# Optimization experiments

Measured on AMD Instinct MI355X. Metric: run time of the kernel, lower is better.

The kernel has to match this reference:

```python
import jax, jax.numpy as jnp
import numpy as np

D_MODEL = 96
D_STATE = 6
D_CONV = 9
D_INNER = 2 * D_MODEL          # expand = 2
DT_RANK = (D_MODEL + 15) // 16  # ceil(d_model/16) = 6
DIM_IN = 64
DIM_OUT = 64
BATCH = 16
SEQLEN = 4096


def setup_inputs() -> dict:
    key = jax.random.key(0)
    ks = jax.random.split(key, 12)
    def s(k, shape, scale=0.02):
        return jax.random.normal(k, shape, jnp.float32) * scale
    return {
        "x": jax.random.normal(ks[0], (BATCH, SEQLEN, D_MODEL), jnp.float32),
        # Mamba block params
        "in_proj_w": s(ks[1], (2 * D_INNER, D_MODEL)),
        "conv_w": s(ks[2], (D_INNER, D_CONV), 0.1),   # depthwise conv kernel
        "conv_b": jnp.zeros((D_INNER,), jnp.float32),
        "x_proj_w": s(ks[3], (DT_RANK + 2 * D_STATE, D_INNER)),
        "dt_proj_w": s(ks[4], (D_INNER, DT_RANK), 0.1),
        "dt_proj_b": s(ks[5], (D_INNER,), 0.1),
        "A_log": jnp.log(jnp.tile(jnp.arange(1, D_STATE + 1, dtype=jnp.float32), (D_INNER, 1))),
        "D_param": jnp.ones((D_INNER,), jnp.float32),
        "out_proj_w": s(ks[6], (D_MODEL, D_INNER)),
        "norm_w": jnp.ones((D_MODEL,), jnp.float32),  # RMSNorm weight
        # heads
        "out_fc_w": s(ks[7], (DIM_IN, D_MODEL)),
        "out_fc_b": jnp.zeros((DIM_IN,), jnp.float32),
        "mu_w": s(ks[8], (DIM_OUT, DIM_IN)),
        "mu_b": jnp.zeros((DIM_OUT,), jnp.float32),
        "sigma_w": s(ks[9], (DIM_OUT, DIM_IN)),
        "sigma_b": jnp.zeros((DIM_OUT,), jnp.float32),
    }


def _mamba_block(x, in_proj_w, conv_w, conv_b, x_proj_w, dt_proj_w, dt_proj_b,
                 A_log, D_param, out_proj_w):
    Bsz = x.shape[0]
    xz = jnp.einsum('bld,ed->ble', x, in_proj_w)          # (B,L,2*ED)
    xs, z = jnp.split(xz, 2, axis=-1)
    # causal depthwise conv1d (torch pads d_conv-1 both sides then trims right)
    xt = xs.transpose(0, 2, 1)                            # (B,ED,L)
    kern = conv_w[:, None, :]                             # (ED,1,K)
    xc = jax.lax.conv_general_dilated(xt, kern, window_strides=(1,),
                                      padding=[(D_CONV - 1, 0)],
                                      feature_group_count=D_INNER)
    xc = (xc + conv_b[None, :, None]).transpose(0, 2, 1)  # (B,L,ED)
    xc = jax.nn.silu(xc)
    dbc = jnp.einsum('ble,fe->blf', xc, x_proj_w)         # (B,L,dt_rank+2N)
    delta_r = dbc[..., :DT_RANK]
    Bm = dbc[..., DT_RANK:DT_RANK + D_STATE]              # (B,L,N)
    Cm = dbc[..., DT_RANK + D_STATE:]                     # (B,L,N)
    delta = jax.nn.softplus(jnp.einsum('blr,er->ble', delta_r, dt_proj_w) + dt_proj_b)
    A = -jnp.exp(A_log)                                   # (ED,N)
    deltaA = jnp.exp(delta[..., None] * A)                # (B,L,ED,N)
    BX = (delta * xc)[..., None] * Bm[:, :, None, :]      # (B,L,ED,N)

    def step(h, inputs):
        dA, bx = inputs
        h = dA * h + bx
        return h, h

    h0 = jnp.zeros((Bsz, D_INNER, D_STATE), x.dtype)
    _, hs = jax.lax.scan(step, h0, (deltaA.swapaxes(0, 1), BX.swapaxes(0, 1)))
    y = jnp.einsum('lben,bln->ble', hs, Cm)               # (B,L,ED)
    y = y + D_param * xc
    y = y * jax.nn.silu(z)
    return jnp.einsum('ble,de->bld', y, out_proj_w)       # (B,L,D)


def reference(x, in_proj_w, conv_w, conv_b, x_proj_w, dt_proj_w, dt_proj_b,
              A_log, D_param, out_proj_w, norm_w,
              out_fc_w, out_fc_b, mu_w, mu_b, sigma_w, sigma_b):
    # residual block: x + mixer(RMSNorm(x))   (dropout is identity at eval)
    h = x * jax.lax.rsqrt(jnp.mean(x * x, axis=-1, keepdims=True) + 1e-5) * norm_w
    out = x + _mamba_block(h, in_proj_w, conv_w, conv_b, x_proj_w,
                           dt_proj_w, dt_proj_b, A_log, D_param, out_proj_w)
    e = out.mean(axis=1)                                  # (B,D)
    feat = jax.nn.elu(jnp.tanh(e @ out_fc_w.T + out_fc_b))
    mu = feat @ mu_w.T + mu_b
    sigma = jax.nn.elu(feat @ sigma_w.T + sigma_b) + 1.0 + 1e-14
    return (feat, mu, sigma)
```

## Files before the change

kernel.cpp:

```cpp
#include <hip/hip_runtime.h>
#include <math.h>

#define BATCH 16
#define SEQLEN 4096
#define D_MODEL 96
#define D_STATE 6
#define D_CONV 9
#define D_INNER 192
#define DT_RANK 6
#define NPOS (BATCH * SEQLEN)

#define NC2 128
#define CT2 (SEQLEN / NC2)
#define NSEG 16
#define CPS (NC2 / NSEG)

#define OFF_XS    0L
#define OFF_Z     (OFF_XS   + (long)NPOS * 96)
#define OFF_OUT4  (OFF_Z    + (long)NPOS * 96)
#define OFF_SEG   (OFF_OUT4 + (long)BATCH * NC2 * 5 * 192 * 4)
#define OFF_XPART (OFF_SEG  + (long)BATCH * NSEG * 5 * 192 * 4)

typedef short v8s __attribute__((ext_vector_type(8)));
typedef float v4f __attribute__((ext_vector_type(4)));

__device__ __forceinline__ float silu_fast(float v) {
    return __fdividef(v, 1.0f + __expf(-v));
}
__device__ __forceinline__ float softplus_fast(float v) {
    return (v > 20.0f) ? v : __logf(1.0f + __expf(v));
}
__device__ __forceinline__ float eluf(float v) {
    return (v > 0.0f) ? v : expm1f(v);
}
__device__ __forceinline__ unsigned int pack_bf16(float a, float b) {
    unsigned int ua = __float_as_uint(a), ub = __float_as_uint(b);
    ua += 0x7FFFu + ((ua >> 16) & 1u);
    ub += 0x7FFFu + ((ub >> 16) & 1u);
    return (ua >> 16) | (ub & 0xFFFF0000u);
}
__device__ __forceinline__ unsigned short bf16h(float v) {
    unsigned int u = __float_as_uint(v);
    u += 0x7FFFu + ((u >> 16) & 1u);
    return (unsigned short)(u >> 16);
}
__device__ __forceinline__ float bf2f(unsigned short h) {
    return __uint_as_float(((unsigned int)h) << 16);
}

#define TP1 64
__global__ __launch_bounds__(256, 2) void k1_rmsnorm_inproj(
    const float* __restrict__ x, const float* __restrict__ W,
    const float* __restrict__ norm_w,
    unsigned short* __restrict__ xs, unsigned short* __restrict__ z,
    float* __restrict__ xpart)
{
    __shared__ unsigned int s_ovl[7680];
    __shared__ unsigned int s_hA[64 * 52];
    __shared__ float s_part[TP1][4];
    __shared__ float s_scale[TP1];
    float* hRow = (float*)s_ovl;
    unsigned int* WB = s_ovl;

    const int tid = threadIdx.x;
    const long p0 = (long)blockIdx.x * TP1;

    {
        const float4* x4 = (const float4*)&x[p0 * 96];
        for (int i = tid; i < TP1 * 24; i += 256) {
            int p = i / 24, dq = i - p * 24;
            float4 v = x4[i];
            float* hr = &hRow[p * 101 + dq * 4];
            hr[0] = v.x; hr[1] = v.y; hr[2] = v.z; hr[3] = v.w;
        }
    }
    __syncthreads();

    {
        int p = tid >> 2, g = tid & 3;
        float ss = 0.0f;
        for (int d = g; d < 96; d += 4) { float v = hRow[p * 101 + d]; ss += v * v; }
        s_part[p][g] = ss;
    }
    __syncthreads();

    if (tid < TP1) {
        float ss = s_part[tid][0] + s_part[tid][1] + s_part[tid][2] + s_part[tid][3];
        s_scale[tid] = 1.0f / sqrtf(ss / 96.0f + 1e-5f);
    } else if (tid < TP1 + 96) {
        int d = tid - TP1;
        float s = 0.0f;
        for (int p = 0; p < TP1; p++) s += hRow[p * 101 + d];
        xpart[(long)blockIdx.x * 96 + d] = s;
    }
    __syncthreads();

    {
        const float2* nw2 = (const float2*)norm_w;
        for (int i = tid; i < TP1 * 48; i += 256) {
            int p = i / 48, dp = i - p * 48;
            float sc = s_scale[p];
            float2 nv = nw2[dp];
            float v0 = hRow[p * 101 + 2 * dp]     * sc * nv.x;
            float v1 = hRow[p * 101 + 2 * dp + 1] * sc * nv.y;
            s_hA[p * 52 + dp] = pack_bf16(v0, v1);
        }
    }

    const int wave = tid >> 6, lane = tid & 63;
    const int quad = lane >> 4, ln = lane & 15;
    const int n0 = wave * 96;

    v4f acc[4][6];
#pragma unroll
    for (int mt = 0; mt < 4; mt++)
#pragma unroll
        for (int nt = 0; nt < 6; nt++) acc[mt][nt] = (v4f){0.f, 0.f, 0.f, 0.f};

    for (int kc = 0; kc < 3; kc++) {
        __syncthreads();
        for (int i = tid; i < 384 * 16; i += 256) {
            int j = i >> 4, kp = i & 15;
            const float2 wv = *(const float2*)&W[j * 96 + kc * 32 + 2 * kp];
            WB[j * 20 + kp] = pack_bf16(wv.x, wv.y);
        }
        __syncthreads();

        v8s bfh[4];
#pragma unroll
        for (int mt = 0; mt < 4; mt++)
            bfh[mt] = *(const v8s*)&s_hA[(mt * 16 + ln) * 52 + kc * 16 + quad * 4];
#pragma unroll
        for (int nt = 0; nt < 6; nt++) {
            v8s aw = *(const v8s*)&WB[(n0 + nt * 16 + ln) * 20 + quad * 4];
#pragma unroll
            for (int mt = 0; mt < 4; mt++)
                acc[mt][nt] = __builtin_amdgcn_mfma_f32_16x16x32_bf16(
                    aw, bfh[mt], acc[mt][nt], 0, 0, 0);
        }
    }

    unsigned short* dst = (wave < 2) ? xs : z;
    const int jb = (wave & 1) * 96;
#pragma unroll
    for (int mt = 0; mt < 4; mt++) {
        long pos = p0 + mt * 16 + ln;
#pragma unroll
        for (int nt = 0; nt < 6; nt++) {
            uint2 v;
            v.x = pack_bf16(acc[mt][nt][0], acc[mt][nt][1]);
            v.y = pack_bf16(acc[mt][nt][2], acc[mt][nt][3]);
            *(uint2*)&dst[pos * D_INNER + jb + nt * 16 + quad * 4] = v;
        }
    }
}

#define SXSTR 200
__global__ __launch_bounds__(192, 4) void k2f_conv_scan(
    const unsigned short* __restrict__ xs, const unsigned short* __restrict__ z,
    const float* __restrict__ conv_w, const float* __restrict__ conv_b,
    const float* __restrict__ x_proj_w,
    const float* __restrict__ dt_w, const float* __restrict__ dt_b,
    const float* __restrict__ A_log, const float* __restrict__ D_param,
    float4* __restrict__ out4)
{
    __shared__ unsigned short sxc[CT2 * SXSTR];
    __shared__ unsigned short sxpB[18 * SXSTR];
    __shared__ float sMeta[CT2][20];
    const int e = threadIdx.x;
    const int c = blockIdx.x & (NC2 - 1);
    const int b = blockIdx.x >> 7;
    const int l0 = c * CT2;
    const long brow = (long)b * SEQLEN;

    {
        unsigned int* xpB = (unsigned int*)sxpB;
        for (int i = e; i < 18 * 96; i += 192) {
            int f = i / 96, kp = i - f * 96;
            const float2 wv = *(const float2*)&x_proj_w[f * 192 + 2 * kp];
            xpB[f * 100 + kp] = pack_bf16(wv.x, wv.y);
        }
    }

    float cw[D_CONV];
#pragma unroll
    for (int k = 0; k < D_CONV; k++) cw[k] = conv_w[e * D_CONV + k];
    const float cb = conv_b[e];
    float win[D_CONV];
#pragma unroll
    for (int k = 0; k < 8; k++) {
        int ll = l0 - 8 + k;
        win[k] = (ll >= 0) ? bf2f(xs[(brow + ll) * D_INNER + e]) : 0.0f;
    }
#pragma unroll
    for (int r = 0; r < CT2; r++) {
        win[8] = bf2f(xs[(brow + l0 + r) * D_INNER + e]);
        float s = cb;
#pragma unroll
        for (int k = 0; k < D_CONV; k++) s += win[k] * cw[k];
        sxc[r * SXSTR + e] = bf16h(silu_fast(s));
#pragma unroll
        for (int k = 0; k < 8; k++) win[k] = win[k + 1];
    }

    const unsigned short* zp = &z[(brow + l0) * D_INNER + e];
    float zv[CT2];
#pragma unroll
    for (int t = 0; t < CT2; t++) zv[t] = bf2f(zp[(long)t * D_INNER]);
    __syncthreads();

    {
        const int wave = e >> 6, lane = e & 63;
        const int quad = lane >> 4, ln = lane & 15;
        if (wave < 2) {
            const int mt = wave;
            const int r1 = (ln < 2) ? 16 + ln : 0;
            v4f dacc[2];
            dacc[0] = (v4f){0.f, 0.f, 0.f, 0.f};
            dacc[1] = (v4f){0.f, 0.f, 0.f, 0.f};
#pragma unroll
            for (int kc = 0; kc < 6; kc++) {
                v8s af  = *(const v8s*)&sxc[(mt * 16 + ln) * SXSTR + kc * 32 + quad * 8];
                v8s bf0 = *(const v8s*)&sxpB[ln * SXSTR + kc * 32 + quad * 8];
                v8s bf1 = *(const v8s*)&sxpB[r1 * SXSTR + kc * 32 + quad * 8];
                dacc[0] = __builtin_amdgcn_mfma_f32_16x16x32_bf16(af, bf0, dacc[0], 0, 0, 0);
                dacc[1] = __builtin_amdgcn_mfma_f32_16x16x32_bf16(af, bf1, dacc[1], 0, 0, 0);
            }
#pragma unroll
            for (int nt = 0; nt < 2; nt++) {
                int f = nt * 16 + ln;
                if (f < 18) {
                    int col = (f < 6) ? f : f + 2;
#pragma unroll
                    for (int r = 0; r < 4; r++)
                        sMeta[mt * 16 + quad * 4 + r][col] = dacc[nt][r];
                }
            }
        }
    }
    __syncthreads();

    float a[D_STATE];
#pragma unroll
    for (int n = 0; n < D_STATE; n++) a[n] = -__expf(A_log[e * D_STATE + n]);
    float dtw[DT_RANK];
#pragma unroll
    for (int q = 0; q < DT_RANK; q++) dtw[q] = dt_w[e * DT_RANK + q];
    const float dtb = dt_b[e];
    const float Dv = D_param[e];
    const float a0 = a[0];

    bool pok = true;
#pragma unroll
    for (int n = 1; n < D_STATE; n++)
        pok = pok && (fabsf(a[n] - (float)(n + 1) * a0)
                      <= 1e-4f * (float)(n + 1) * fabsf(a0));
    unsigned long long pmask = __ballot(pok);

    float S[D_STATE], G[D_STATE];
#pragma unroll
    for (int n = 0; n < D_STATE; n++) { S[n] = 0.0f; G[n] = 0.0f; }
    float ysum0 = 0.0f;

    if (pmask == 0xFFFFFFFFFFFFFFFFull) {
        float Pa = 1.0f;
#pragma unroll 2
        for (int t = 0; t < CT2; t++) {
            const float4* m4 = (const float4*)&sMeta[t][0];
            float4 m0 = m4[0], m1 = m4[1], mB0 = m4[2], mB1 = m4[3], mC = m4[4];
            float Bv[6] = {mB0.x, mB0.y, mB0.z, mB0.w, mB1.x, mB1.y};
            float Cv[6] = {mB1.z, mB1.w, mC.x, mC.y, mC.z, mC.w};
            float dr = dtb + m0.x * dtw[0] + m0.y * dtw[1] + m0.z * dtw[2]
                     + m0.w * dtw[3] + m1.x * dtw[4] + m1.y * dtw[5];
            float dl = softplus_fast(dr);
            float xv = bf2f(sxc[t * SXSTR + e]);
            float zw = silu_fast(zv[t]);
            float dx = dl * xv;
            float y = Dv * xv;
            float E = __expf(dl * a0);
            Pa *= E;
            float dA = E, Pn = Pa;
#pragma unroll
            for (int n = 0; n < D_STATE; n++) {
                S[n] = dA * S[n] + dx * Bv[n];
                y += S[n] * Cv[n];
                G[n] += zw * Pn * Cv[n];
                dA *= E;
                Pn *= Pa;
            }
            ysum0 += zw * y;
        }
        long ob = (long)(b * NC2 + c) * 5 * 192 + e;
        float P1 = Pa, P2 = P1 * Pa, P3 = P2 * Pa, P4 = P3 * Pa, P5 = P4 * Pa, P6 = P5 * Pa;
        float4 q0, q1, q2, q3, q4;
        q0.x=P1; q0.y=P2; q0.z=P3; q0.w=P4;
        q1.x=P5; q1.y=P6; q1.z=S[0]; q1.w=S[1];
        q2.x=S[2]; q2.y=S[3]; q2.z=S[4]; q2.w=S[5];
        q3.x=G[0]; q3.y=G[1]; q3.z=G[2]; q3.w=G[3];
        q4.x=G[4]; q4.y=G[5]; q4.z=ysum0; q4.w=0.0f;
        out4[ob          ] = q0;
        out4[ob + 192    ] = q1;
        out4[ob + 2 * 192] = q2;
        out4[ob + 3 * 192] = q3;
        out4[ob + 4 * 192] = q4;
    } else {
        float P[D_STATE];
#pragma unroll
        for (int n = 0; n < D_STATE; n++) P[n] = 1.0f;
#pragma unroll 2
        for (int t = 0; t < CT2; t++) {
            const float4* m4 = (const float4*)&sMeta[t][0];
            float4 m0 = m4[0], m1 = m4[1], mB0 = m4[2], mB1 = m4[3], mC = m4[4];
            float Bv[6] = {mB0.x, mB0.y, mB0.z, mB0.w, mB1.x, mB1.y};
            float Cv[6] = {mB1.z, mB1.w, mC.x, mC.y, mC.z, mC.w};
            float dr = dtb + m0.x * dtw[0] + m0.y * dtw[1] + m0.z * dtw[2]
                     + m0.w * dtw[3] + m1.x * dtw[4] + m1.y * dtw[5];
            float dl = softplus_fast(dr);
            float xv = bf2f(sxc[t * SXSTR + e]);
            float zw = silu_fast(zv[t]);
            float dx = dl * xv;
            float y = Dv * xv;
#pragma unroll
            for (int n = 0; n < D_STATE; n++) {
                float dA = __expf(dl * a[n]);
                S[n] = dA * S[n] + dx * Bv[n];
                P[n] *= dA;
                y += S[n] * Cv[n];
                G[n] += zw * P[n] * Cv[n];
            }
            ysum0 += zw * y;
        }
        long ob = (long)(b * NC2 + c) * 5 * 192 + e;
        float4 q0, q1, q2, q3, q4;
        q0.x=P[0]; q0.y=P[1]; q0.z=P[2]; q0.w=P[3];
        q1.x=P[4]; q1.y=P[5]; q1.z=S[0]; q1.w=S[1];
        q2.x=S[2]; q2.y=S[3]; q2.z=S[4]; q2.w=S[5];
        q3.x=G[0]; q3.y=G[1]; q3.z=G[2]; q3.w=G[3];
        q4.x=G[4]; q4.y=G[5]; q4.z=ysum0; q4.w=0.0f;
        out4[ob          ] = q0;
        out4[ob + 192    ] = q1;
        out4[ob + 2 * 192] = q2;
        out4[ob + 3 * 192] = q3;
        out4[ob + 4 * 192] = q4;
    }
}

__global__ __launch_bounds__(192) void k4_seg(
    const float4* __restrict__ out4, float4* __restrict__ seg4)
{
    const int e = threadIdx.x;
    const int s = blockIdx.x & (NSEG - 1);
    const int b = blockIdx.x >> 4;

    float H[D_STATE], Gq[D_STATE], Pp[D_STATE];
#pragma unroll
    for (int n = 0; n < D_STATE; n++) { H[n] = 0.0f; Gq[n] = 0.0f; Pp[n] = 1.0f; }
    float yb = 0.0f;
#pragma unroll 2
    for (int cc = 0; cc < CPS; cc++) {
        int c = s * CPS + cc;
        long ob = (long)(b * NC2 + c) * 5 * 192 + e;
        float4 q0 = out4[ob];
        float4 q1 = out4[ob + 192];
        float4 q2 = out4[ob + 2 * 192];
        float4 q3 = out4[ob + 3 * 192];
        float4 q4 = out4[ob + 4 * 192];
        float Pv[6] = {q0.x, q0.y, q0.z, q0.w, q1.x, q1.y};
        float Sv[6] = {q1.z, q1.w, q2.x, q2.y, q2.z, q2.w};
        float Gv[6] = {q3.x, q3.y, q3.z, q3.w, q4.x, q4.y};
        float g = 0.0f;
#pragma unroll
        for (int n = 0; n < D_STATE; n++) g += Gv[n] * H[n];
        yb += q4.z + g;
#pragma unroll
        for (int n = 0; n < D_STATE; n++) {
            Gq[n] += Gv[n] * Pp[n];
            H[n] = Pv[n] * H[n] + Sv[n];
            Pp[n] *= Pv[n];
        }
    }
    long sb = (long)(b * NSEG + s) * 5 * 192 + e;
    float4 q0, q1, q2, q3, q4;
    q0.x=Pp[0]; q0.y=Pp[1]; q0.z=Pp[2]; q0.w=Pp[3];
    q1.x=Pp[4]; q1.y=Pp[5]; q1.z=H[0]; q1.w=H[1];
    q2.x=H[2]; q2.y=H[3]; q2.z=H[4]; q2.w=H[5];
    q3.x=Gq[0]; q3.y=Gq[1]; q3.z=Gq[2]; q3.w=Gq[3];
    q4.x=Gq[4]; q4.y=Gq[5]; q4.z=yb; q4.w=0.0f;
    seg4[sb          ] = q0;
    seg4[sb + 192    ] = q1;
    seg4[sb + 2 * 192] = q2;
    seg4[sb + 3 * 192] = q3;
    seg4[sb + 4 * 192] = q4;
}

__global__ __launch_bounds__(192) void k4_head(
    const float4* __restrict__ seg4, const float* __restrict__ xpart,
    const float* __restrict__ Wout,
    const float* __restrict__ fc_w, const float* __restrict__ fc_b,
    const float* __restrict__ mu_w, const float* __restrict__ mu_b,
    const float* __restrict__ sg_w, const float* __restrict__ sg_b,
    float* __restrict__ out)
{
    __shared__ float ybar[D_INNER];
    __shared__ float sxb[D_MODEL];
    __shared__ float evec[D_MODEL];
    __shared__ float feat_s[64];
    const int e = threadIdx.x;
    const int b = blockIdx.x;

    float H[D_STATE];
#pragma unroll
    for (int n = 0; n < D_STATE; n++) H[n] = 0.0f;
    float yb = 0.0f;
#pragma unroll 4
    for (int s = 0; s < NSEG; s++) {
        long ob = (long)(b * NSEG + s) * 5 * 192 + e;
        float4 q0 = seg4[ob];
        float4 q1 = seg4[ob + 192];
        float4 q2 = seg4[ob + 2 * 192];
        float4 q3 = seg4[ob + 3 * 192];
        float4 q4 = seg4[ob + 4 * 192];
        float Pv[6] = {q0.x, q0.y, q0.z, q0.w, q1.x, q1.y};
        float Sv[6] = {q1.z, q1.w, q2.x, q2.y, q2.z, q2.w};
        float Gv[6] = {q3.x, q3.y, q3.z, q3.w, q4.x, q4.y};
        float g = 0.0f;
#pragma unroll
        for (int n = 0; n < D_STATE; n++) g += Gv[n] * H[n];
        yb += q4.z + g;
#pragma unroll
        for (int n = 0; n < D_STATE; n++) H[n] = Pv[n] * H[n] + Sv[n];
    }
    ybar[e] = yb;

    if (e < D_MODEL) {
        const float* xp = &xpart[(long)b * 64 * 96 + e];
        float s = 0.0f;
        for (int t = 0; t < 64; t++) s += xp[t * 96];
        sxb[e] = s;
    }
    __syncthreads();

    if (e < D_MODEL) {
        float s = sxb[e];
        const float* wrow = &Wout[e * D_INNER];
        for (int e2 = 0; e2 < D_INNER; e2++) s += ybar[e2] * wrow[e2];
        evec[e] = s / (float)SEQLEN;
    }
    __syncthreads();

    if (e < 64) {
        float s = fc_b[e];
        const float* wrow = &fc_w[e * D_MODEL];
        for (int d = 0; d < D_MODEL; d++) s += evec[d] * wrow[d];
        float f = eluf(tanhf(s));
        feat_s[e] = f;
        out[b * 64 + e] = f;
    }
    __syncthreads();

    if (e < 64) {
        float smu = mu_b[e], ssg = sg_b[e];
        const float* mrow = &mu_w[e * 64];
        const float* srow = &sg_w[e * 64];
        for (int i = 0; i < 64; i++) {
            smu += feat_s[i] * mrow[i];
            ssg += feat_s[i] * srow[i];
        }
        out[1024 + b * 64 + e] = smu;
        out[2048 + b * 64 + e] = eluf(ssg) + 1.0f + 1e-14f;
    }
}

extern "C" void kernel_launch(void* const* d_in, const int* in_sizes, int n_in,
                              void* d_out, int out_size, void* d_ws, size_t ws_size,
                              hipStream_t stream) {
    const float* x         = (const float*)d_in[0];
    const float* in_proj_w = (const float*)d_in[1];
    const float* conv_w    = (const float*)d_in[2];
    const float* conv_b    = (const float*)d_in[3];
    const float* x_proj_w  = (const float*)d_in[4];
    const float* dt_proj_w = (const float*)d_in[5];
    const float* dt_proj_b = (const float*)d_in[6];
    const float* A_log     = (const float*)d_in[7];
    const float* D_param   = (const float*)d_in[8];
    const float* out_proj_w= (const float*)d_in[9];
    const float* norm_w    = (const float*)d_in[10];
    const float* out_fc_w  = (const float*)d_in[11];
    const float* out_fc_b  = (const float*)d_in[12];
    const float* mu_w      = (const float*)d_in[13];
    const float* mu_b      = (const float*)d_in[14];
    const float* sigma_w   = (const float*)d_in[15];
    const float* sigma_b   = (const float*)d_in[16];
    float* ws = (float*)d_ws;
    float* out = (float*)d_out;

    k1_rmsnorm_inproj<<<NPOS / TP1, 256, 0, stream>>>(
        x, in_proj_w, norm_w,
        (unsigned short*)(ws + OFF_XS), (unsigned short*)(ws + OFF_Z),
        ws + OFF_XPART);

    k2f_conv_scan<<<BATCH * NC2, 192, 0, stream>>>(
        (const unsigned short*)(ws + OFF_XS), (const unsigned short*)(ws + OFF_Z),
        conv_w, conv_b, x_proj_w,
        dt_proj_w, dt_proj_b, A_log, D_param,
        (float4*)(ws + OFF_OUT4));

    k4_seg<<<BATCH * NSEG, 192, 0, stream>>>(
        (const float4*)(ws + OFF_OUT4), (float4*)(ws + OFF_SEG));

    k4_head<<<BATCH, 192, 0, stream>>>(
        (const float4*)(ws + OFF_SEG), ws + OFF_XPART, out_proj_w,
        out_fc_w, out_fc_b, mu_w, mu_b, sigma_w, sigma_b, out);
}
```

Baseline: 206.9 us.

## Fuse RMSNorm+in_proj GEMM into conv/scan kernel, dropping xs/z global round-trip

Merges the RMSNorm/in_proj kernel into the conv+scan kernel: each block recomputes the in_proj GEMM for its 32-position chunk plus an 8-row halo, keeping xs and z in shared memory. This removes the bf16 xs/z global writes and re-reads and one kernel launch. In exchange, each block redoes the halo rows' projection, reloads and converts the full in_proj weight per block, and runs with more shared memory and a lower occupancy bound.

```diff
diff --git a/kernel.cpp b/kernel.cpp
--- a/kernel.cpp
+++ b/kernel.cpp
@@ -15,9 +15,7 @@
 #define NSEG 16
 #define CPS (NC2 / NSEG)
 
-#define OFF_XS    0L
-#define OFF_Z     (OFF_XS   + (long)NPOS * 96)
-#define OFF_OUT4  (OFF_Z    + (long)NPOS * 96)
+#define OFF_OUT4  0L
 #define OFF_SEG   (OFF_OUT4 + (long)BATCH * NC2 * 5 * 192 * 4)
 #define OFF_XPART (OFF_SEG  + (long)BATCH * NSEG * 5 * 192 * 4)
 
@@ -48,198 +46,201 @@
     return __uint_as_float(((unsigned int)h) << 16);
 }
 
-#define TP1 64
-__global__ __launch_bounds__(256, 2) void k1_rmsnorm_inproj(
+#define SXSTR 200
+__global__ __launch_bounds__(192, 2) void ka_fused(
     const float* __restrict__ x, const float* __restrict__ W,
     const float* __restrict__ norm_w,
-    unsigned short* __restrict__ xs, unsigned short* __restrict__ z,
-    float* __restrict__ xpart)
+    const float* __restrict__ conv_w, const float* __restrict__ conv_b,
+    const float* __restrict__ x_proj_w,
+    const float* __restrict__ dt_w, const float* __restrict__ dt_b,
+    const float* __restrict__ A_log, const float* __restrict__ D_param,
+    float4* __restrict__ out4, float* __restrict__ xpart)
 {
-    __shared__ unsigned int s_ovl[7680];
-    __shared__ unsigned int s_hA[64 * 52];
-    __shared__ float s_part[TP1][4];
-    __shared__ float s_scale[TP1];
-    float* hRow = (float*)s_ovl;
-    unsigned int* WB = s_ovl;
+    __shared__ unsigned short sxs[40 * SXSTR];
+    __shared__ unsigned short zL[32 * SXSTR];
+    __shared__ unsigned int   s_wb[4040];
+    __shared__ unsigned int   s_hN[40 * 52];
+    __shared__ float s_scale[40];
+    __shared__ float s_part[40][4];
+
+    float* hRow = (float*)s_wb;
+    unsigned int* WB = s_wb;
+    unsigned short* sxpB = (unsigned short*)s_wb;
+    float* sMeta = (float*)s_hN;
 
     const int tid = threadIdx.x;
-    const long p0 = (long)blockIdx.x * TP1;
+    const int c = blockIdx.x & (NC2 - 1);
+    const int b = blockIdx.x >> 7;
+    const int l0 = c * CT2;
+    const long brow = (long)b * SEQLEN;
 
     {
-        const float4* x4 = (const float4*)&x[p0 * 96];
-        for (int i = tid; i < TP1 * 24; i += 256) {
+        const float4* x4 = (const float4*)&x[0];
+        long gbase = (brow + l0 - 8) * 24;
+        for (int i = tid; i < 40 * 24; i += 192) {
             int p = i / 24, dq = i - p * 24;
-            float4 v = x4[i];
+            float4 v = {0.f, 0.f, 0.f, 0.f};
+            if (l0 - 8 + p >= 0) v = x4[gbase + i];
             float* hr = &hRow[p * 101 + dq * 4];
             hr[0] = v.x; hr[1] = v.y; hr[2] = v.z; hr[3] = v.w;
         }
     }
     __syncthreads();
 
-    {
+    if (tid < 160) {
         int p = tid >> 2, g = tid & 3;
         float ss = 0.0f;
         for (int d = g; d < 96; d += 4) { float v = hRow[p * 101 + d]; ss += v * v; }
         s_part[p][g] = ss;
     }
     __syncthreads();
-
-    if (tid < TP1) {
+    if (tid < 40) {
         float ss = s_part[tid][0] + s_part[tid][1] + s_part[tid][2] + s_part[tid][3];
         s_scale[tid] = 1.0f / sqrtf(ss / 96.0f + 1e-5f);
-    } else if (tid < TP1 + 96) {
-        int d = tid - TP1;
+    } else if (tid < 40 + 96) {
+        int d = tid - 40;
         float s = 0.0f;
-        for (int p = 0; p < TP1; p++) s += hRow[p * 101 + d];
-        xpart[(long)blockIdx.x * 96 + d] = s;
+        for (int p = 8; p < 40; p++) s += hRow[p * 101 + d];
+        xpart[(long)(b * NC2 + c) * 96 + d] = s;
     }
     __syncthreads();
 
     {
         const float2* nw2 = (const float2*)norm_w;
-        for (int i = tid; i < TP1 * 48; i += 256) {
+        for (int i = tid; i < 40 * 48; i += 192) {
             int p = i / 48, dp = i - p * 48;
             float sc = s_scale[p];
             float2 nv = nw2[dp];
             float v0 = hRow[p * 101 + 2 * dp]     * sc * nv.x;
             float v1 = hRow[p * 101 + 2 * dp + 1] * sc * nv.y;
-            s_hA[p * 52 + dp] = pack_bf16(v0, v1);
+            s_hN[p * 52 + dp] = pack_bf16(v0, v1);
         }
     }
 
     const int wave = tid >> 6, lane = tid & 63;
     const int quad = lane >> 4, ln = lane & 15;
-    const int n0 = wave * 96;
-
-    v4f acc[4][6];
-#pragma unroll
-    for (int mt = 0; mt < 4; mt++)
-#pragma unroll
-        for (int nt = 0; nt < 6; nt++) acc[mt][nt] = (v4f){0.f, 0.f, 0.f, 0.f};
+
+    v4f accX[3][4], accZ[3][4];
+#pragma unroll
+    for (int mt = 0; mt < 3; mt++)
+#pragma unroll
+        for (int nt = 0; nt < 4; nt++) {
+            accX[mt][nt] = (v4f){0.f, 0.f, 0.f, 0.f};
+            accZ[mt][nt] = (v4f){0.f, 0.f, 0.f, 0.f};
+        }
 
     for (int kc = 0; kc < 3; kc++) {
-        __syncthreads();
-        for (int i = tid; i < 384 * 16; i += 256) {
-            int j = i >> 4, kp = i & 15;
-            const float2 wv = *(const float2*)&W[j * 96 + kc * 32 + 2 * kp];
-            WB[j * 20 + kp] = pack_bf16(wv.x, wv.y);
-        }
-        __syncthreads();
-
-        v8s bfh[4];
-#pragma unroll
-        for (int mt = 0; mt < 4; mt++)
-            bfh[mt] = *(const v8s*)&s_hA[(mt * 16 + ln) * 52 + kc * 16 + quad * 4];
-#pragma unroll
-        for (int nt = 0; nt < 6; nt++) {
-            v8s aw = *(const v8s*)&WB[(n0 + nt * 16 + ln) * 20 + quad * 4];
-#pragma unroll
-            for (int mt = 0; mt < 4; mt++)
-                acc[mt][nt] = __builtin_amdgcn_mfma_f32_16x16x32_bf16(
-                    aw, bfh[mt], acc[mt][nt], 0, 0, 0);
-        }
-    }
-
-    unsigned short* dst = (wave < 2) ? xs : z;
-    const int jb = (wave & 1) * 96;
-#pragma unroll
-    for (int mt = 0; mt < 4; mt++) {
-        long pos = p0 + mt * 16 + ln;
-#pragma unroll
-        for (int nt = 0; nt < 6; nt++) {
-            uint2 v;
-            v.x = pack_bf16(acc[mt][nt][0], acc[mt][nt][1]);
-            v.y = pack_bf16(acc[mt][nt][2], acc[mt][nt][3]);
-            *(uint2*)&dst[pos * D_INNER + jb + nt * 16 + quad * 4] = v;
-        }
-    }
-}
-
-#define SXSTR 200
-__global__ __launch_bounds__(192, 4) void k2f_conv_scan(
-    const unsigned short* __restrict__ xs, const unsigned short* __restrict__ z,
-    const float* __restrict__ conv_w, const float* __restrict__ conv_b,
-    const float* __restrict__ x_proj_w,
-    const float* __restrict__ dt_w, const float* __restrict__ dt_b,
-    const float* __restrict__ A_log, const float* __restrict__ D_param,
-    float4* __restrict__ out4)
-{
-    __shared__ unsigned short sxc[CT2 * SXSTR];
-    __shared__ unsigned short sxpB[18 * SXSTR];
-    __shared__ float sMeta[CT2][20];
-    const int e = threadIdx.x;
-    const int c = blockIdx.x & (NC2 - 1);
-    const int b = blockIdx.x >> 7;
-    const int l0 = c * CT2;
-    const long brow = (long)b * SEQLEN;
+#pragma unroll
+        for (int half = 0; half < 2; half++) {
+            __syncthreads();
+            for (int i = tid; i < 192 * 16; i += 192) {
+                int j = i >> 4, kp = i & 15;
+                const float2 wv = *(const float2*)&W[(half * 192 + j) * 96 + kc * 32 + 2 * kp];
+                WB[j * 20 + kp] = pack_bf16(wv.x, wv.y);
+            }
+            __syncthreads();
+
+            v8s af[3];
+#pragma unroll
+            for (int mt = 0; mt < 3; mt++) {
+                int pr = mt * 16 + ln;
+                if (pr > 39) pr = 39;
+                af[mt] = *(const v8s*)&s_hN[pr * 52 + kc * 16 + quad * 4];
+            }
+#pragma unroll
+            for (int nt = 0; nt < 4; nt++) {
+                int jn = wave * 64 + nt * 16 + ln;
+                v8s bw = *(const v8s*)&WB[jn * 20 + quad * 4];
+                if (half == 0) {
+#pragma unroll
+                    for (int mt = 0; mt < 3; mt++)
+                        accX[mt][nt] = __builtin_amdgcn_mfma_f32_16x16x32_bf16(
+                            af[mt], bw, accX[mt][nt], 0, 0, 0);
+                } else {
+#pragma unroll
+                    for (int mt = 0; mt < 3; mt++)
+                        accZ[mt][nt] = __builtin_amdgcn_mfma_f32_16x16x32_bf16(
+                            af[mt], bw, accZ[mt][nt], 0, 0, 0);
+                }
+            }
+        }
+    }
+
+#pragma unroll
+    for (int mt = 0; mt < 3; mt++) {
+#pragma unroll
+        for (int nt = 0; nt < 4; nt++) {
+            int j = wave * 64 + nt * 16 + ln;
+#pragma unroll
+            for (int r = 0; r < 4; r++) {
+                int p = mt * 16 + quad * 4 + r;
+                if (p < 40) {
+                    sxs[p * SXSTR + j] = bf16h(accX[mt][nt][r]);
+                    if (p >= 8) zL[(p - 8) * SXSTR + j] = bf16h(accZ[mt][nt][r]);
+                }
+            }
+        }
+    }
+    __syncthreads();
 
     {
         unsigned int* xpB = (unsigned int*)sxpB;
-        for (int i = e; i < 18 * 96; i += 192) {
+        for (int i = tid; i < 18 * 96; i += 192) {
             int f = i / 96, kp = i - f * 96;
             const float2 wv = *(const float2*)&x_proj_w[f * 192 + 2 * kp];
-            xpB[f * 100 + kp] = pack_bf16(wv.x, wv.y);
-        }
-    }
-
-    float cw[D_CONV];
-#pragma unroll
-    for (int k = 0; k < D_CONV; k++) cw[k] = conv_w[e * D_CONV + k];
-    const float cb = conv_b[e];
-    float win[D_CONV];
-#pragma unroll
-    for (int k = 0; k < 8; k++) {
-        int ll = l0 - 8 + k;
-        win[k] = (ll >= 0) ? bf2f(xs[(brow + ll) * D_INNER + e]) : 0.0f;
-    }
-#pragma unroll
-    for (int r = 0; r < CT2; r++) {
-        win[8] = bf2f(xs[(brow + l0 + r) * D_INNER + e]);
-        float s = cb;
-#pragma unroll
-        for (int k = 0; k < D_CONV; k++) s += win[k] * cw[k];
-        sxc[r * SXSTR + e] = bf16h(silu_fast(s));
-#pragma unroll
-        for (int k = 0; k < 8; k++) win[k] = win[k + 1];
-    }
-
-    const unsigned short* zp = &z[(brow + l0) * D_INNER + e];
-    float zv[CT2];
-#pragma unroll
-    for (int t = 0; t < CT2; t++) zv[t] = bf2f(zp[(long)t * D_INNER]);
-    __syncthreads();
-
+            xpB[f * (SXSTR / 2) + kp] = pack_bf16(wv.x, wv.y);
+        }
+    }
     {
-        const int wave = e >> 6, lane = e & 63;
-        const int quad = lane >> 4, ln = lane & 15;
-        if (wave < 2) {
-            const int mt = wave;
-            const int r1 = (ln < 2) ? 16 + ln : 0;
-            v4f dacc[2];
-            dacc[0] = (v4f){0.f, 0.f, 0.f, 0.f};
-            dacc[1] = (v4f){0.f, 0.f, 0.f, 0.f};
-#pragma unroll
-            for (int kc = 0; kc < 6; kc++) {
-                v8s af  = *(const v8s*)&sxc[(mt * 16 + ln) * SXSTR + kc * 32 + quad * 8];
-                v8s bf0 = *(const v8s*)&sxpB[ln * SXSTR + kc * 32 + quad * 8];
-                v8s bf1 = *(const v8s*)&sxpB[r1 * SXSTR + kc * 32 + quad * 8];
-                dacc[0] = __builtin_amdgcn_mfma_f32_16x16x32_bf16(af, bf0, dacc[0], 0, 0, 0);
-                dacc[1] = __builtin_amdgcn_mfma_f32_16x16x32_bf16(af, bf1, dacc[1], 0, 0, 0);
-            }
-#pragma unroll
-            for (int nt = 0; nt < 2; nt++) {
-                int f = nt * 16 + ln;
-                if (f < 18) {
-                    int col = (f < 6) ? f : f + 2;
-#pragma unroll
-                    for (int r = 0; r < 4; r++)
-                        sMeta[mt * 16 + quad * 4 + r][col] = dacc[nt][r];
-                }
-            }
-        }
-    }
-    __syncthreads();
-
+        const int e = tid;
+        float cw[D_CONV];
+#pragma unroll
+        for (int k = 0; k < D_CONV; k++) cw[k] = conv_w[e * D_CONV + k];
+        const float cb = conv_b[e];
+        float win[D_CONV];
+#pragma unroll
+        for (int k = 0; k < 8; k++) win[k] = bf2f(sxs[k * SXSTR + e]);
+#pragma unroll
+        for (int r = 0; r < CT2; r++) {
+            win[8] = bf2f(sxs[(r + 8) * SXSTR + e]);
+            float s = cb;
+#pragma unroll
+            for (int k = 0; k < D_CONV; k++) s += win[k] * cw[k];
+            sxs[r * SXSTR + e] = bf16h(silu_fast(s));
+#pragma unroll
+            for (int k = 0; k < 8; k++) win[k] = win[k + 1];
+        }
+    }
+    __syncthreads();
+
+    if (wave < 2) {
+        const int mt = wave;
+        const int r1 = (ln < 2) ? 16 + ln : 0;
+        v4f dacc[2];
+        dacc[0] = (v4f){0.f, 0.f, 0.f, 0.f};
+        dacc[1] = (v4f){0.f, 0.f, 0.f, 0.f};
+#pragma unroll
+        for (int kc = 0; kc < 6; kc++) {
+            v8s af  = *(const v8s*)&sxs[(mt * 16 + ln) * SXSTR + kc * 32 + quad * 8];
+            v8s bf0 = *(const v8s*)&sxpB[ln * SXSTR + kc * 32 + quad * 8];
+            v8s bf1 = *(const v8s*)&sxpB[r1 * SXSTR + kc * 32 + quad * 8];
+            dacc[0] = __builtin_amdgcn_mfma_f32_16x16x32_bf16(af, bf0, dacc[0], 0, 0, 0);
+            dacc[1] = __builtin_amdgcn_mfma_f32_16x16x32_bf16(af, bf1, dacc[1], 0, 0, 0);
+        }
+#pragma unroll
+        for (int nt = 0; nt < 2; nt++) {
+            int f = nt * 16 + ln;
+            if (f < 18) {
+                int col = (f < 6) ? f : f + 2;
+#pragma unroll
+                for (int r = 0; r < 4; r++)
+                    sMeta[(mt * 16 + quad * 4 + r) * 20 + col] = dacc[nt][r];
+            }
+        }
+    }
+    __syncthreads();
+
+    const int e = tid;
     float a[D_STATE];
 #pragma unroll
     for (int n = 0; n < D_STATE; n++) a[n] = -__expf(A_log[e * D_STATE + n]);
@@ -266,15 +267,15 @@
         float Pa = 1.0f;
 #pragma unroll 2
         for (int t = 0; t < CT2; t++) {
-            const float4* m4 = (const float4*)&sMeta[t][0];
+            const float4* m4 = (const float4*)&sMeta[t * 20];
             float4 m0 = m4[0], m1 = m4[1], mB0 = m4[2], mB1 = m4[3], mC = m4[4];
             float Bv[6] = {mB0.x, mB0.y, mB0.z, mB0.w, mB1.x, mB1.y};
             float Cv[6] = {mB1.z, mB1.w, mC.x, mC.y, mC.z, mC.w};
             float dr = dtb + m0.x * dtw[0] + m0.y * dtw[1] + m0.z * dtw[2]
                      + m0.w * dtw[3] + m1.x * dtw[4] + m1.y * dtw[5];
             float dl = softplus_fast(dr);
-            float xv = bf2f(sxc[t * SXSTR + e]);
-            float zw = silu_fast(zv[t]);
+            float xv = bf2f(sxs[t * SXSTR + e]);
+            float zw = silu_fast(bf2f(zL[t * SXSTR + e]));
             float dx = dl * xv;
             float y = Dv * xv;
             float E = __expf(dl * a0);
@@ -309,15 +310,15 @@
         for (int n = 0; n < D_STATE; n++) P[n] = 1.0f;
 #pragma unroll 2
         for (int t = 0; t < CT2; t++) {
-            const float4* m4 = (const float4*)&sMeta[t][0];
+            const float4* m4 = (const float4*)&sMeta[t * 20];
             float4 m0 = m4[0], m1 = m4[1], mB0 = m4[2], mB1 = m4[3], mC = m4[4];
             float Bv[6] = {mB0.x, mB0.y, mB0.z, mB0.w, mB1.x, mB1.y};
             float Cv[6] = {mB1.z, mB1.w, mC.x, mC.y, mC.z, mC.w};
             float dr = dtb + m0.x * dtw[0] + m0.y * dtw[1] + m0.z * dtw[2]
                      + m0.w * dtw[3] + m1.x * dtw[4] + m1.y * dtw[5];
             float dl = softplus_fast(dr);
-            float xv = bf2f(sxc[t * SXSTR + e]);
-            float zw = silu_fast(zv[t]);
+            float xv = bf2f(sxs[t * SXSTR + e]);
+            float zw = silu_fast(bf2f(zL[t * SXSTR + e]));
             float dx = dl * xv;
             float y = Dv * xv;
 #pragma unroll
@@ -433,9 +434,9 @@
     ybar[e] = yb;
 
     if (e < D_MODEL) {
-        const float* xp = &xpart[(long)b * 64 * 96 + e];
+        const float* xp = &xpart[(long)b * NC2 * 96 + e];
         float s = 0.0f;
-        for (int t = 0; t < 64; t++) s += xp[t * 96];
+        for (int t = 0; t < NC2; t++) s += xp[t * 96];
         sxb[e] = s;
     }
     __syncthreads();
@@ -494,16 +495,10 @@
     float* ws = (float*)d_ws;
     float* out = (float*)d_out;
 
-    k1_rmsnorm_inproj<<<NPOS / TP1, 256, 0, stream>>>(
-        x, in_proj_w, norm_w,
-        (unsigned short*)(ws + OFF_XS), (unsigned short*)(ws + OFF_Z),
-        ws + OFF_XPART);
-
-    k2f_conv_scan<<<BATCH * NC2, 192, 0, stream>>>(
-        (const unsigned short*)(ws + OFF_XS), (const unsigned short*)(ws + OFF_Z),
-        conv_w, conv_b, x_proj_w,
+    ka_fused<<<BATCH * NC2, 192, 0, stream>>>(
+        x, in_proj_w, norm_w, conv_w, conv_b, x_proj_w,
         dt_proj_w, dt_proj_b, A_log, D_param,
-        (float4*)(ws + OFF_OUT4));
+        (float4*)(ws + OFF_OUT4), ws + OFF_XPART);
 
     k4_seg<<<BATCH * NSEG, 192, 0, stream>>>(
         (const float4*)(ws + OFF_OUT4), (float4*)(ws + OFF_SEG));
```

New measurement: 237.6 us. +14.8%, slower.
